# Kernel tuning notes

Measured on AMD Instinct MI355X. Metric: run time of the kernel, lower is better.

## Reference

```python
import jax, jax.numpy as jnp
import numpy as np

B, S, HID = 2, 2048, 2560
NH, NKV, HD = 8, 4, 256
Q_SIZE, KV_SIZE = NH * HD, NKV * HD
SCALE = 256.0 ** -0.5
SLIDING_WINDOW = 1024 - 1  # config.sliding_window - 1
ROPE_BASE = 10000.0
EPS = 1e-6


def rmsnorm(x, w, eps=EPS):
    xf = x.astype(jnp.float32)
    out = xf * jax.lax.rsqrt(jnp.mean(xf * xf, axis=-1, keepdims=True) + eps)
    return (out * (1.0 + w.astype(jnp.float32))).astype(x.dtype)


def apply_rope(x, positions):
    # x: [B,S,H,D], neox style (rotate halves)
    d = x.shape[-1]
    inv_freq = 1.0 / (ROPE_BASE ** (jnp.arange(0, d, 2, dtype=jnp.float32) / d))
    freqs = positions.astype(jnp.float32)[..., None] * inv_freq  # [B,S,d/2]
    cos = jnp.cos(freqs)[:, :, None, :]
    sin = jnp.sin(freqs)[:, :, None, :]
    x1, x2 = x[..., : d // 2], x[..., d // 2:]
    return jnp.concatenate([x1 * cos - x2 * sin, x2 * cos + x1 * sin], axis=-1).astype(x.dtype)


def setup_inputs() -> dict:
    key = jax.random.key(0)
    ks = jax.random.split(key, 4)
    positions = jnp.broadcast_to(jnp.arange(S, dtype=jnp.int32)[None, :], (B, S))
    hidden_states = jax.random.normal(ks[0], (B, S, HID), dtype=jnp.float32)
    attention_mask = jnp.ones((B, S), dtype=jnp.int32)
    Wqkv = jax.random.normal(ks[1], (HID, Q_SIZE + 2 * KV_SIZE), dtype=jnp.float32) * (HID ** -0.5)
    Wo = jax.random.normal(ks[2], (Q_SIZE, HID), dtype=jnp.float32) * (Q_SIZE ** -0.5)
    q_norm_w = jnp.zeros((HD,), dtype=jnp.float32)
    k_norm_w = jnp.zeros((HD,), dtype=jnp.float32)
    return {"positions": positions, "hidden_states": hidden_states,
            "attention_mask": attention_mask, "Wqkv": Wqkv, "Wo": Wo,
            "q_norm_w": q_norm_w, "k_norm_w": k_norm_w}


def reference(positions, hidden_states, attention_mask, Wqkv, Wo, q_norm_w, k_norm_w):
    b, s, _ = hidden_states.shape
    qkv = hidden_states @ Wqkv
    q, k, v = jnp.split(qkv, [Q_SIZE, Q_SIZE + KV_SIZE], axis=-1)
    q = q.reshape(b, s, NH, HD)
    k = k.reshape(b, s, NKV, HD)
    v = v.reshape(b, s, NKV, HD)
    q = rmsnorm(q, q_norm_w)
    k = rmsnorm(k, k_norm_w)
    q = apply_rope(q, positions)
    k = apply_rope(k, positions)

    # additive mask, replicating source exactly
    idx = jnp.arange(s)
    causal = idx[None, :] > idx[:, None]             # triu(diag=1)
    too_far = (idx[None, :] - idx[:, None]) > SLIDING_WINDOW
    base_mask = causal | too_far                      # [S,S]
    key_pad = attention_mask.astype(bool) == False    # [B,S]
    masked = base_mask[None, None, :, :] | key_pad[:, None, None, :]  # [B,1,S,S]
    add_mask = jnp.where(masked, -jnp.inf, 0.0).astype(jnp.float32)

    # GQA: group queries over kv heads
    g = NH // NKV
    qg = q.reshape(b, s, NKV, g, HD)
    scores = jnp.einsum('bsmgd,btmd->bmgst', qg, k) * SCALE  # [B,NKV,g,S,S]
    scores = scores + add_mask[:, :, None, :, :]
    probs = jax.nn.softmax(scores, axis=-1)
    out = jnp.einsum('bmgst,btmd->bsmgd', probs, v)           # [B,S,NKV,g,HD]
    out = out.reshape(b, s, NH * HD)
    return out @ Wo
```

## Files before the change

kernel.cpp:

```cpp
#include <hip/hip_runtime.h>
#include <stdint.h>

#define S_LEN 2048
#define BATCH 2
#define HIDDEN 2560
#define NH 8
#define NKV 4
#define HD 256
#define QSZ (NH*HD)
#define NQKV 4096
#define MROWS (BATCH*S_LEN)
#define SCALE_ATT 0.0625f

using bf16x8 = __attribute__((__ext_vector_type__(8))) __bf16;
using f32x4  = __attribute__((__ext_vector_type__(4))) float;
using s16x8  = __attribute__((__ext_vector_type__(8))) short;

union B8u { s16x8 s; bf16x8 b; };
union I4B8 { int4 i; bf16x8 b; };

__device__ __forceinline__ unsigned short f2bf(float x){
  unsigned u = __float_as_uint(x);
  u += 0x7fffu + ((u >> 16) & 1u);
  return (unsigned short)(u >> 16);
}
__device__ __forceinline__ float bf2f(unsigned short h){
  return __uint_as_float(((unsigned)h) << 16);
}
__device__ __forceinline__ bf16x8 ld_bf8(const unsigned short* p){
  B8u u; u.s = *reinterpret_cast<const s16x8*>(p); return u.b;
}
__device__ __forceinline__ f32x4 mfma16(bf16x8 a, bf16x8 b, f32x4 c){
  return __builtin_amdgcn_mfma_f32_16x16x32_bf16(a, b, c, 0, 0, 0);
}
__device__ __forceinline__ void gload16(const void* g, void* l){
  __builtin_amdgcn_global_load_lds((const __attribute__((address_space(1))) void*)g,
                                   (__attribute__((address_space(3))) void*)l,
                                   16, 0, 0);
}
__device__ __forceinline__ int cvtpk(float lo, float hi){
  int r;
  asm("v_cvt_pk_bf16_f32 %0, %1, %2" : "=v"(r) : "v"(lo), "v"(hi));
  return r;
}

__global__ __launch_bounds__(256) void cast_bf16_kernel(
    const float* __restrict__ in, unsigned short* __restrict__ out, int n)
{
  int i = (blockIdx.x * 256 + threadIdx.x) * 4;
  if (i < n){
    float4 v = *reinterpret_cast<const float4*>(in + i);
    ushort4 o;
    o.x = f2bf(v.x); o.y = f2bf(v.y); o.z = f2bf(v.z); o.w = f2bf(v.w);
    *reinterpret_cast<ushort4*>(out + i) = o;
  }
}

__global__ __launch_bounds__(256) void tcast_kernel(
    const float* __restrict__ in, unsigned short* __restrict__ out, int R, int C)
{
  __shared__ float t[32][33];
  int c0 = blockIdx.x * 32, r0 = blockIdx.y * 32;
  int tx = threadIdx.x & 31, ty = threadIdx.x >> 5;
#pragma unroll
  for (int ii = 0; ii < 4; ii++)
    t[ty + ii*8][tx] = in[(size_t)(r0 + ty + ii*8) * C + c0 + tx];
  __syncthreads();
#pragma unroll
  for (int ii = 0; ii < 4; ii++)
    out[(size_t)(c0 + ty + ii*8) * R + r0 + tx] = f2bf(t[tx][ty + ii*8]);
}

template<int BF16OUT>
__global__ __launch_bounds__(512, 2) void gemm256_kernel(
    const unsigned short* __restrict__ A,
    const unsigned short* __restrict__ BT,
    void* __restrict__ Cv,
    int N, int K, int nbn)
{
  __shared__ unsigned short Ab[2][256 * 64];
  __shared__ unsigned short Bb[2][256 * 64];

  const int tid  = threadIdx.x;
  const int lane = tid & 63;
  const int wid  = tid >> 6;
  const int wm = wid >> 2, wn = wid & 3;
  const int lq = lane & 15, lk = lane >> 4;

  const int cpx = gridDim.x >> 3;
  const int wg  = (blockIdx.x & 7) * cpx + (blockIdx.x >> 3);
  const int bm = wg / nbn, bn = wg % nbn;

  const int l8 = lane >> 3;
  const int sl = ((lane & 7) ^ l8) * 8;
  const unsigned short* agS = A  + (size_t)(bm*256 + wid*16 + l8) * K + sl;
  const unsigned short* bgS = BT + (size_t)(bn*256 + wid*16 + l8) * K + sl;

  f32x4 acc[4][4][2] = {};
  bf16x8 a[4][2], b[2][2];

#define STA(c, h, tt) do {                                                    \
    unsigned short* d = &Ab[c][(h)*8192 + wid*1024];                          \
    const unsigned short* s = agS + (size_t)(h)*128*K + (size_t)(tt)*64;      \
    gload16(s, d); gload16(s + 8*(size_t)K, d + 512);                         \
  } while (0)
#define STB(c, h, tt) do {                                                    \
    unsigned short* d = &Bb[c][(h)*8192 + wid*1024];                          \
    const unsigned short* s = bgS + (size_t)(h)*128*K + (size_t)(tt)*64;      \
    gload16(s, d); gload16(s + 8*(size_t)K, d + 512);                         \
  } while (0)
#define LDA(qa) do {                                                          \
    _Pragma("unroll") for (int m = 0; m < 4; m++)                             \
    _Pragma("unroll") for (int kk = 0; kk < 2; kk++)                          \
      a[m][kk] = ld_bf8(&Ab[cur][((qa)*128 + wm*64 + m*16 + lq)*64            \
                                 + (((kk*4 + lk) ^ (lq & 7)) << 3)]);         \
  } while (0)
#define LDB(qb) do {                                                          \
    _Pragma("unroll") for (int n = 0; n < 2; n++)                             \
    _Pragma("unroll") for (int kk = 0; kk < 2; kk++)                          \
      b[n][kk] = ld_bf8(&Bb[cur][((qb)*128 + wn*32 + n*16 + lq)*64            \
                                 + (((kk*4 + lk) ^ (lq & 7)) << 3)]);         \
  } while (0)
#define MM(qi) do {                                                           \
    __builtin_amdgcn_s_setprio(1);                                            \
    _Pragma("unroll") for (int m = 0; m < 4; m++)                             \
    _Pragma("unroll") for (int n = 0; n < 2; n++)                             \
    _Pragma("unroll") for (int kk = 0; kk < 2; kk++)                          \
      acc[qi][m][n] = mfma16(a[m][kk], b[n][kk], acc[qi][m][n]);              \
    __builtin_amdgcn_s_setprio(0);                                            \
  } while (0)
#define BARR __builtin_amdgcn_s_barrier()
#define VM(n) asm volatile("s_waitcnt vmcnt(" #n ")" ::: "memory")

  STA(0, 0, 0); STB(0, 0, 0); STB(0, 1, 0); STA(0, 1, 0);
  VM(4); BARR;

  const int NT = K >> 6;
  for (int t = 0; t < NT - 1; ++t){
    const int cur = t & 1, nxt = cur ^ 1;
    LDA(0); LDB(0); STA(nxt, 0, t+1);
    BARR; MM(0); VM(4); BARR;
    LDB(1);         STB(nxt, 0, t+1);
    BARR; MM(1); VM(4); BARR;
    LDA(1);         STB(nxt, 1, t+1);
    BARR; MM(2);        BARR;
    LDB(0);         STA(nxt, 1, t+1);
    BARR; MM(3); VM(4); BARR;
  }
  {
    const int cur = (NT - 1) & 1;
    LDA(0); LDB(0); BARR; MM(0); VM(2); BARR;
    LDB(1);         BARR; MM(1); VM(0); BARR;
    LDA(1);         BARR; MM(2);        BARR;
    LDB(0);         BARR; MM(3);        BARR;
  }
#undef STA
#undef STB
#undef LDA
#undef LDB
#undef MM
#undef BARR
#undef VM

#pragma unroll
  for (int qi = 0; qi < 4; qi++){
    const int qa = qi >> 1;
    const int qb = (qi ^ (qi >> 1)) & 1;
    const int r0 = bm*256 + qa*128 + wm*64;
    const int c0 = bn*256 + qb*128 + wn*32;
#pragma unroll
    for (int m = 0; m < 4; m++)
#pragma unroll
      for (int n = 0; n < 2; n++)
#pragma unroll
        for (int i = 0; i < 4; i++){
          const size_t idx = (size_t)(r0 + m*16 + lk*4 + i) * N + (c0 + n*16 + lq);
          if (BF16OUT) ((unsigned short*)Cv)[idx] = f2bf(acc[qi][m][n][i]);
          else         ((float*)Cv)[idx]          = acc[qi][m][n][i];
        }
  }
}

__global__ __launch_bounds__(256) void normrope_kernel(
    const unsigned short* __restrict__ qkv,
    const int* __restrict__ positions,
    const float* __restrict__ qw, const float* __restrict__ kw,
    unsigned short* __restrict__ qB,
    unsigned short* __restrict__ kB,
    unsigned short* __restrict__ vT)
{
  const int s = blockIdx.x, b = blockIdx.y;
  const int lane = threadIdx.x & 63, wid = threadIdx.x >> 6;
  const unsigned short* row = qkv + (size_t)(b * S_LEN + s) * NQKV;
  const float fpos = (float)positions[b * S_LEN + s];

#pragma unroll
  for (int t = 0; t < 4; t++){
    const int seg = t * 4 + wid;
    const int base = seg * HD;
    float x0 = bf2f(row[base + lane]);
    float x1 = bf2f(row[base + lane + 64]);
    float x2 = bf2f(row[base + lane + 128]);
    float x3 = bf2f(row[base + lane + 192]);
    if (seg >= 12){
      const int mh = seg - 12;
      unsigned short* vb = vT + (size_t)(b * NKV + mh) * HD * S_LEN + s;
      vb[(size_t)(lane      ) * S_LEN] = f2bf(x0);
      vb[(size_t)(lane +  64) * S_LEN] = f2bf(x1);
      vb[(size_t)(lane + 128) * S_LEN] = f2bf(x2);
      vb[(size_t)(lane + 192) * S_LEN] = f2bf(x3);
    } else {
      const float* w = (seg < 8) ? qw : kw;
      float ssq = x0*x0 + x1*x1 + x2*x2 + x3*x3;
#pragma unroll
      for (int d = 1; d < 64; d <<= 1) ssq += __shfl_xor(ssq, d, 64);
      float rs = rsqrtf(ssq * (1.0f / 256.0f) + 1e-6f);
      float y0 = x0 * rs * (1.0f + w[lane]);
      float y1 = x1 * rs * (1.0f + w[lane + 64]);
      float y2 = x2 * rs * (1.0f + w[lane + 128]);
      float y3 = x3 * rs * (1.0f + w[lane + 192]);
      const float kln = -9.210340371976184f / 128.0f;
      float inv1 = expf((float)lane * kln);
      float inv2 = expf((float)(lane + 64) * kln);
      float s1, c1, s2, c2;
      sincosf(fpos * inv1, &s1, &c1);
      sincosf(fpos * inv2, &s2, &c2);
      float o0 = y0 * c1 - y2 * s1;
      float o2 = y2 * c1 + y0 * s1;
      float o1 = y1 * c2 - y3 * s2;
      float o3 = y3 * c2 + y1 * s2;
      unsigned short* dst = (seg < 8)
        ? qB + ((size_t)(b * NH  +  seg     ) * S_LEN + s) * HD
        : kB + ((size_t)(b * NKV + (seg - 8)) * S_LEN + s) * HD;
      dst[lane      ] = f2bf(o0);
      dst[lane +  64] = f2bf(o1);
      dst[lane + 128] = f2bf(o2);
      dst[lane + 192] = f2bf(o3);
    }
  }
}

__global__ void maskbits_kernel(const int* __restrict__ amask, unsigned* __restrict__ bm,
                                int* __restrict__ ctr)
{
  int t = threadIdx.x;
  int b = t >> 6, tile = t & 63;
  unsigned m = 0;
  for (int j = 0; j < 32; j++)
    m |= (amask[b * S_LEN + tile * 32 + j] != 0 ? 1u : 0u) << j;
  bm[t] = m;
  if (t < 8) ctr[t] = 0;
}

__global__ __launch_bounds__(256) void attn_kernel(
    const unsigned short* __restrict__ qB,
    const unsigned short* __restrict__ kB,
    const unsigned short* __restrict__ vT,
    const unsigned* __restrict__ bmG,
    unsigned short* __restrict__ attnO,
    int* __restrict__ ctr)
{
  __shared__ unsigned short Kb[4][32 * 256];
  __shared__ unsigned short Vb[4][256 * 32];
  __shared__ unsigned bm_lds[64];
  __shared__ int s_idx;

  const int tid  = threadIdx.x;
  const int lane = tid & 63, wid = tid >> 6;
  const int c  = blockIdx.x & 7;
  const int mh = c & 3, b = c >> 2;
  const int h  = mh * 2 + (wid >> 1);
  const int lq = lane & 15, lk = lane >> 4;

  if (tid < 64) bm_lds[tid] = bmG[(b << 6) + tid];

  const unsigned short* kbase = kB + (size_t)(b * NKV + mh) * S_LEN * HD;
  const unsigned short* vbase = vT + (size_t)(b * NKV + mh) * HD * S_LEN;
  const int krow0 = wid * 2 + (lane >> 5);
  const int kgsrc = (lane & 31) ^ (krow0 & 7);
  const unsigned short* kg0 = kbase + (size_t)krow0 * HD + kgsrc * 8;
  const int vd0 = wid * 16 + (lane >> 2);
  const int vgsrc = (lane & 3) ^ ((lane >> 3) & 3);
  const unsigned short* vg0 = vbase + (size_t)vd0 * S_LEN + vgsrc * 8;

#define STAGE_K(buf, ktv)                                                      \
  do {                                                                         \
    _Pragma("unroll")                                                          \
    for (int r = 0; r < 4; r++)                                                \
      gload16(kg0 + (size_t)(ktv) * HD + r * (8 * HD),                         \
              &Kb[buf][wid * 512 + r * 2048]);                                 \
  } while (0)
#define STAGE_V(buf, ktv)                                                      \
  do {                                                                         \
    _Pragma("unroll")                                                          \
    for (int r = 0; r < 4; r++)                                                \
      gload16(vg0 + (ktv) + (size_t)r * (64 * S_LEN),                          \
              &Vb[buf][wid * 512 + r * 2048]);                                 \
  } while (0)

  for (;;){
    if (tid == 0) s_idx = atomicAdd(&ctr[c], 1);
    __syncthreads();
    const int idx = s_idx;
    __syncthreads();
    if (idx >= 64) break;
    const int qt = 63 - idx;

    const int q0 = qt * 32 + (wid & 1) * 16;
    const int q  = q0 + lq;

    const unsigned short* qbase = qB + ((size_t)(b * NH + h) * S_LEN + q0 + lq) * HD + lk * 8;
    bf16x8 aq[8];
#pragma unroll
    for (int ks = 0; ks < 8; ks++) aq[ks] = ld_bf8(qbase + ks * 32);
    asm volatile("s_waitcnt vmcnt(0)" ::: "memory");

    float mi = -__builtin_inff(), li = 0.f;
    f32x4 oacc[16] = {};

    STAGE_K(0, 0); STAGE_V(0, 0);
    if (qt >= 1){ STAGE_K(1, 32); STAGE_V(1, 32); }
    if (qt >= 2){ STAGE_K(2, 64); STAGE_V(2, 64); }
    if (qt >= 3){ STAGE_K(3, 96); STAGE_V(3, 96); }

    const int npairs = (qt >> 1) + 1;
    for (int p = 0; p < npairs; ++p){
      const int ktA = p * 64;
      const int ktB = ktA + 32;
      const bool hasB = (2*p + 1 <= qt);
      const int bufA = (2*p) & 3, bufB = (2*p + 1) & 3;

      const int ahead = qt - 2*p - 1;
      if (ahead >= 2)      asm volatile("s_waitcnt vmcnt(16)" ::: "memory");
      else if (ahead == 1) asm volatile("s_waitcnt vmcnt(8)"  ::: "memory");
      else                 asm volatile("s_waitcnt vmcnt(0)"  ::: "memory");
      __syncthreads();

      f32x4 sA0 = {0.f,0.f,0.f,0.f}, sA1 = {0.f,0.f,0.f,0.f};
      f32x4 sB0 = {0.f,0.f,0.f,0.f}, sB1 = {0.f,0.f,0.f,0.f};
      if (hasB){
#pragma unroll
        for (int ks = 0; ks < 8; ks++){
          const int slot = (((ks * 4 + lk) ^ (lq & 7)) << 3);
          bf16x8 kA0 = ld_bf8(&Kb[bufA][lq * 256 + slot]);
          bf16x8 kA1 = ld_bf8(&Kb[bufA][(16 + lq) * 256 + slot]);
          bf16x8 kB0 = ld_bf8(&Kb[bufB][lq * 256 + slot]);
          bf16x8 kB1 = ld_bf8(&Kb[bufB][(16 + lq) * 256 + slot]);
          sA0 = mfma16(kA0, aq[ks], sA0);
          sA1 = mfma16(kA1, aq[ks], sA1);
          sB0 = mfma16(kB0, aq[ks], sB0);
          sB1 = mfma16(kB1, aq[ks], sB1);
        }
      } else {
#pragma unroll
        for (int ks = 0; ks < 8; ks++){
          const int slot = (((ks * 4 + lk) ^ (lq & 7)) << 3);
          bf16x8 kA0 = ld_bf8(&Kb[bufA][lq * 256 + slot]);
          bf16x8 kA1 = ld_bf8(&Kb[bufA][(16 + lq) * 256 + slot]);
          sA0 = mfma16(kA0, aq[ks], sA0);
          sA1 = mfma16(kA1, aq[ks], sA1);
        }
      }

      const unsigned mA = bm_lds[ktA >> 5];
      const unsigned mB = bm_lds[(ktB >> 5) & 63];
      const int koff = lk * 4;
      float vA0[4], vA1[4], vB0[4], vB1[4];
#pragma unroll
      for (int j2 = 0; j2 < 4; j2++){
        const bool a0 = (ktA + koff + j2 <= q)      && ((mA >> (koff + j2)) & 1u);
        const bool a1 = (ktA + 16 + koff + j2 <= q) && ((mA >> (16 + koff + j2)) & 1u);
        vA0[j2] = a0 ? sA0[j2] * SCALE_ATT : -__builtin_inff();
        vA1[j2] = a1 ? sA1[j2] * SCALE_ATT : -__builtin_inff();
      }
      if (hasB){
#pragma unroll
        for (int j2 = 0; j2 < 4; j2++){
          const bool b0 = (ktB + koff + j2 <= q)      && ((mB >> (koff + j2)) & 1u);
          const bool b1 = (ktB + 16 + koff + j2 <= q) && ((mB >> (16 + koff + j2)) & 1u);
          vB0[j2] = b0 ? sB0[j2] * SCALE_ATT : -__builtin_inff();
          vB1[j2] = b1 ? sB1[j2] * SCALE_ATT : -__builtin_inff();
        }
      } else {
#pragma unroll
        for (int j2 = 0; j2 < 4; j2++){ vB0[j2] = -__builtin_inff(); vB1[j2] = -__builtin_inff(); }
      }
      float tm = fmaxf(fmaxf(fmaxf(vA0[0], vA0[1]), fmaxf(vA0[2], vA0[3])),
                       fmaxf(fmaxf(vA1[0], vA1[1]), fmaxf(vA1[2], vA1[3])));
      if (hasB){
        float tb = fmaxf(fmaxf(fmaxf(vB0[0], vB0[1]), fmaxf(vB0[2], vB0[3])),
                         fmaxf(fmaxf(vB1[0], vB1[1]), fmaxf(vB1[2], vB1[3])));
        tm = fmaxf(tm, tb);
      }
      tm = fmaxf(tm, __shfl_xor(tm, 16, 64));
      tm = fmaxf(tm, __shfl_xor(tm, 32, 64));

      float pA0[4], pA1[4], pB0[4], pB1[4];
      if (__all(tm <= mi + 8.0f)){
        const float mns = fmaxf(mi, -1e30f);
#pragma unroll
        for (int j2 = 0; j2 < 4; j2++){
          pA0[j2] = __expf(vA0[j2] - mns); pA1[j2] = __expf(vA1[j2] - mns);
          pB0[j2] = __expf(vB0[j2] - mns); pB1[j2] = __expf(vB1[j2] - mns);
        }
        float rs = (pA0[0]+pA0[1])+(pA0[2]+pA0[3])+(pA1[0]+pA1[1])+(pA1[2]+pA1[3])
                 + (pB0[0]+pB0[1])+(pB0[2]+pB0[3])+(pB1[0]+pB1[1])+(pB1[2]+pB1[3]);
        rs += __shfl_xor(rs, 16, 64);
        rs += __shfl_xor(rs, 32, 64);
        li += rs;
      } else {
        const float mn  = fmaxf(mi, tm);
        const float mns = fmaxf(mn, -1e30f);
#pragma unroll
        for (int j2 = 0; j2 < 4; j2++){
          pA0[j2] = __expf(vA0[j2] - mns); pA1[j2] = __expf(vA1[j2] - mns);
          pB0[j2] = __expf(vB0[j2] - mns); pB1[j2] = __expf(vB1[j2] - mns);
        }
        const float a_ = __expf(mi - mns);
        float rs = (pA0[0]+pA0[1])+(pA0[2]+pA0[3])+(pA1[0]+pA1[1])+(pA1[2]+pA1[3])
                 + (pB0[0]+pB0[1])+(pB0[2]+pB0[3])+(pB1[0]+pB1[1])+(pB1[2]+pB1[3]);
        rs += __shfl_xor(rs, 16, 64);
        rs += __shfl_xor(rs, 32, 64);
        li = li * a_ + rs;
        mi = mn;
        float av[4];
#pragma unroll
        for (int i = 0; i < 4; i++)
          av[i] = __shfl(a_, (lane & 48) | (lk * 4 + i), 64);
#pragma unroll
        for (int db = 0; db < 16; db++){
          f32x4 o = oacc[db];
#pragma unroll
          for (int i = 0; i < 4; i++) o[i] *= av[i];
          oacc[db] = o;
        }
      }

      const int sA_ = (((lk & 1) * 2) << 4) | lq;
      const int sB_ = sA_ + 16;
      const bool hi = (lk >= 2);
      I4B8 pauA, pauB;
      {
        const int w0 = cvtpk(pA0[0], pA0[1]), w1 = cvtpk(pA0[2], pA0[3]);
        const int w2 = cvtpk(pA1[0], pA1[1]), w3 = cvtpk(pA1[2], pA1[3]);
        const int a0 = __shfl(w0, sA_, 64), a1 = __shfl(w1, sA_, 64);
        const int b0 = __shfl(w0, sB_, 64), b1 = __shfl(w1, sB_, 64);
        const int c0w = __shfl(w2, sA_, 64), c1w = __shfl(w3, sA_, 64);
        const int d0w = __shfl(w2, sB_, 64), d1w = __shfl(w3, sB_, 64);
        pauA.i.x = hi ? c0w : a0;
        pauA.i.y = hi ? c1w : a1;
        pauA.i.z = hi ? d0w : b0;
        pauA.i.w = hi ? d1w : b1;
      }
      if (hasB){
        const int w0 = cvtpk(pB0[0], pB0[1]), w1 = cvtpk(pB0[2], pB0[3]);
        const int w2 = cvtpk(pB1[0], pB1[1]), w3 = cvtpk(pB1[2], pB1[3]);
        const int a0 = __shfl(w0, sA_, 64), a1 = __shfl(w1, sA_, 64);
        const int b0 = __shfl(w0, sB_, 64), b1 = __shfl(w1, sB_, 64);
        const int c0w = __shfl(w2, sA_, 64), c1w = __shfl(w3, sA_, 64);
        const int d0w = __shfl(w2, sB_, 64), d1w = __shfl(w3, sB_, 64);
        pauB.i.x = hi ? c0w : a0;
        pauB.i.y = hi ? c1w : a1;
        pauB.i.z = hi ? d0w : b0;
        pauB.i.w = hi ? d1w : b1;
      }

      const int vslot = (lk ^ ((lq >> 1) & 3)) << 3;
      if (hasB){
#pragma unroll
        for (int db = 0; db < 16; db++){
          bf16x8 vfA = ld_bf8(&Vb[bufA][(db * 16 + lq) * 32 + vslot]);
          bf16x8 vfB = ld_bf8(&Vb[bufB][(db * 16 + lq) * 32 + vslot]);
          f32x4 o = mfma16(pauA.b, vfA, oacc[db]);
          oacc[db] = mfma16(pauB.b, vfB, o);
        }
      } else {
#pragma unroll
        for (int db = 0; db < 16; db++){
          bf16x8 vfA = ld_bf8(&Vb[bufA][(db * 16 + lq) * 32 + vslot]);
          oacc[db] = mfma16(pauA.b, vfA, oacc[db]);
        }
      }

      __syncthreads();
      if (2*p + 4 <= qt){ STAGE_K(bufA, ktA + 128); STAGE_V(bufA, ktA + 128); }
      if (2*p + 5 <= qt){ STAGE_K(bufB, ktB + 128); STAGE_V(bufB, ktB + 128); }
    }

#pragma unroll
    for (int i = 0; i < 4; i++){
      const float lf = __shfl(li, (lane & 48) | (lk * 4 + i), 64);
      const float inv = 1.0f / lf;
      unsigned short* orow = attnO + (size_t)(b * S_LEN + q0 + lk*4 + i) * QSZ + h * HD + lq;
#pragma unroll
      for (int db = 0; db < 16; db++)
        orow[db * 16] = f2bf(oacc[db][i] * inv);
    }
  }
#undef STAGE_K
#undef STAGE_V
}

extern "C" void kernel_launch(void* const* d_in, const int* in_sizes, int n_in,
                              void* d_out, int out_size, void* d_ws, size_t ws_size,
                              hipStream_t stream)
{
  const int*   positions = (const int*)  d_in[0];
  const float* hidden    = (const float*)d_in[1];
  const int*   amask     = (const int*)  d_in[2];
  const float* Wqkv      = (const float*)d_in[3];
  const float* Wo        = (const float*)d_in[4];
  const float* qw        = (const float*)d_in[5];
  const float* kw        = (const float*)d_in[6];
  float* out = (float*)d_out;

  char* ws = (char*)d_ws;
  unsigned short* hB    = (unsigned short*)(ws);
  unsigned short* attnO = (unsigned short*)(ws);
  unsigned short* WqT   = (unsigned short*)(ws + 20971520);
  unsigned short* WoT   = (unsigned short*)(ws + 41943040);
  unsigned short* qkvB  = (unsigned short*)(ws + 52428800);
  unsigned short* qb    = (unsigned short*)(ws + 119537664);
  unsigned short* kb    = (unsigned short*)(ws + 136314880);
  unsigned short* vt    = (unsigned short*)(ws + 144703488);
  unsigned*       bm    = (unsigned*)     (ws + 153092096);
  int*            ctr   = (int*)          (ws + 153092608);

  cast_bf16_kernel<<<dim3(MROWS * HIDDEN / 1024), 256, 0, stream>>>(hidden, hB, MROWS * HIDDEN);
  tcast_kernel<<<dim3(NQKV / 32, HIDDEN / 32), 256, 0, stream>>>(Wqkv, WqT, HIDDEN, NQKV);
  tcast_kernel<<<dim3(HIDDEN / 32, QSZ / 32), 256, 0, stream>>>(Wo, WoT, QSZ, HIDDEN);
  maskbits_kernel<<<dim3(1), 128, 0, stream>>>(amask, bm, ctr);

  gemm256_kernel<1><<<dim3((MROWS/256) * (NQKV/256)), 512, 0, stream>>>(
      hB, WqT, qkvB, NQKV, HIDDEN, NQKV/256);

  normrope_kernel<<<dim3(S_LEN, BATCH), 256, 0, stream>>>(qkvB, positions, qw, kw, qb, kb, vt);

  attn_kernel<<<dim3(256), 256, 0, stream>>>(qb, kb, vt, bm, attnO, ctr);

  gemm256_kernel<0><<<dim3((MROWS/256) * (HIDDEN/256)), 512, 0, stream>>>(
      attnO, WoT, out, HIDDEN, QSZ, HIDDEN/256);
}
```

Before: 336.4 us.

## Fuse QK RMSNorm, RoPE and V transpose into QKV GEMM epilogue

Removes the separate normrope kernel and the bf16 qkv intermediate. The QKV GEMM epilogue now computes per-row RMS across a 256-wide head tile through an LDS reduction, applies RoPE from a precomputed cos/sin table, and writes q/k/v^T directly. A small ropetab kernel builds the sin/cos tables, and the epilogue stores are scattered 2-byte writes with strided table reads. The goal is to cut a full round trip through memory and a kernel launch, at the cost of a heavier epilogue and more register pressure.

```diff
diff --git a/kernel.cpp b/kernel.cpp
--- a/kernel.cpp
+++ b/kernel.cpp
@@ -24,9 +24,6 @@
   u += 0x7fffu + ((u >> 16) & 1u);
   return (unsigned short)(u >> 16);
 }
-__device__ __forceinline__ float bf2f(unsigned short h){
-  return __uint_as_float(((unsigned)h) << 16);
-}
 __device__ __forceinline__ bf16x8 ld_bf8(const unsigned short* p){
   B8u u; u.s = *reinterpret_cast<const s16x8*>(p); return u.b;
 }
@@ -71,16 +68,38 @@
     out[(size_t)(c0 + ty + ii*8) * R + r0 + tx] = f2bf(t[tx][ty + ii*8]);
 }
 
-template<int BF16OUT>
-__global__ __launch_bounds__(512, 2) void gemm256_kernel(
+__global__ __launch_bounds__(256) void ropetab_kernel(
+    const int* __restrict__ positions, float* __restrict__ ct, float* __restrict__ st)
+{
+  const int cix = blockIdx.x;
+  const int b   = blockIdx.y;
+  const float kln = -9.210340371976184f / 128.0f;
+  const float inv = expf((float)cix * kln);
+  float* cp = ct + ((size_t)b * 128 + cix) * 2048;
+  float* sp = st + ((size_t)b * 128 + cix) * 2048;
+  for (int s = threadIdx.x; s < S_LEN; s += 256){
+    float fpos = (float)positions[b * S_LEN + s];
+    float sv, cv;
+    sincosf(fpos * inv, &sv, &cv);
+    cp[s] = cv;
+    sp[s] = sv;
+  }
+}
+
+__global__ __launch_bounds__(512, 2) void gemm_qkv_kernel(
     const unsigned short* __restrict__ A,
     const unsigned short* __restrict__ BT,
-    void* __restrict__ Cv,
-    int N, int K, int nbn)
+    const float* __restrict__ qw, const float* __restrict__ kw,
+    const float* __restrict__ ct, const float* __restrict__ st,
+    unsigned short* __restrict__ qB,
+    unsigned short* __restrict__ kB,
+    unsigned short* __restrict__ vT)
 {
   __shared__ unsigned short Ab[2][256 * 64];
   __shared__ unsigned short Bb[2][256 * 64];
 
+  const int K = HIDDEN;
+  const int nbn = 16;
   const int tid  = threadIdx.x;
   const int lane = tid & 63;
   const int wid  = tid >> 6;
@@ -162,6 +181,199 @@
 #undef BARR
 #undef VM
 
+  __syncthreads();
+  const int b_  = bm >> 3;
+  const int sb0 = (bm & 7) * 256;
+
+  if (bn >= 12){
+    const int mhv = bn - 12;
+#pragma unroll
+    for (int qi = 0; qi < 4; qi++){
+      const int qa = qi >> 1, qb = (qi ^ (qi >> 1)) & 1;
+#pragma unroll
+      for (int m = 0; m < 4; m++){
+        const int s0 = sb0 + qa*128 + wm*64 + m*16 + lk*4;
+#pragma unroll
+        for (int n = 0; n < 2; n++){
+          const int d = qb*128 + wn*32 + n*16 + lq;
+          ushort4 o;
+          o.x = f2bf(acc[qi][m][n][0]);
+          o.y = f2bf(acc[qi][m][n][1]);
+          o.z = f2bf(acc[qi][m][n][2]);
+          o.w = f2bf(acc[qi][m][n][3]);
+          *reinterpret_cast<ushort4*>(
+              vT + ((size_t)((b_*NKV + mhv)*HD + d))*S_LEN + s0) = o;
+        }
+      }
+    }
+  } else {
+    float* red = (float*)Ab;
+    float part[2][4][4];
+#pragma unroll
+    for (int qa = 0; qa < 2; qa++){
+      const int qiA = qa ? 3 : 0, qiB = qa ? 2 : 1;
+#pragma unroll
+      for (int m = 0; m < 4; m++)
+#pragma unroll
+      for (int i = 0; i < 4; i++){
+        float s = 0.f;
+#pragma unroll
+        for (int n = 0; n < 2; n++)
+          s += acc[qiA][m][n][i]*acc[qiA][m][n][i]
+             + acc[qiB][m][n][i]*acc[qiB][m][n][i];
+        s += __shfl_xor(s, 1, 64);
+        s += __shfl_xor(s, 2, 64);
+        s += __shfl_xor(s, 4, 64);
+        s += __shfl_xor(s, 8, 64);
+        part[qa][m][i] = s;
+      }
+    }
+    if (lq == 0){
+#pragma unroll
+      for (int qa = 0; qa < 2; qa++)
+#pragma unroll
+      for (int m = 0; m < 4; m++)
+#pragma unroll
+      for (int i = 0; i < 4; i++)
+        red[wn*256 + qa*128 + wm*64 + m*16 + lk*4 + i] = part[qa][m][i];
+    }
+    __syncthreads();
+    float rsv[2][4][4];
+#pragma unroll
+    for (int qa = 0; qa < 2; qa++)
+#pragma unroll
+    for (int m = 0; m < 4; m++)
+#pragma unroll
+    for (int i = 0; i < 4; i++){
+      const int row = qa*128 + wm*64 + m*16 + lk*4 + i;
+      float tt = red[row] + red[256 + row] + red[512 + row] + red[768 + row];
+      rsv[qa][m][i] = rsqrtf(tt * (1.0f/256.0f) + 1e-6f);
+    }
+    const float* wv = (bn < 8) ? qw : kw;
+    unsigned short* dstB = (bn < 8)
+      ? qB + ((size_t)(b_*NH  + bn      ) * S_LEN) * HD
+      : kB + ((size_t)(b_*NKV + (bn - 8)) * S_LEN) * HD;
+    const float* ctb = ct + (size_t)b_ * 128 * 2048;
+    const float* stb = st + (size_t)b_ * 128 * 2048;
+#pragma unroll
+    for (int qa = 0; qa < 2; qa++){
+      const int qiA = qa ? 3 : 0, qiB = qa ? 2 : 1;
+#pragma unroll
+      for (int m = 0; m < 4; m++){
+        const int s0 = sb0 + qa*128 + wm*64 + m*16 + lk*4;
+#pragma unroll
+        for (int n = 0; n < 2; n++){
+          const int c0 = wn*32 + n*16 + lq;
+          const float w0 = 1.0f + wv[c0];
+          const float w1 = 1.0f + wv[c0 + 128];
+          const float4 c4 = *reinterpret_cast<const float4*>(ctb + (size_t)c0*2048 + s0);
+          const float4 s4 = *reinterpret_cast<const float4*>(stb + (size_t)c0*2048 + s0);
+#pragma unroll
+          for (int i = 0; i < 4; i++){
+            const float rs_ = rsv[qa][m][i];
+            const float y0 = acc[qiA][m][n][i] * rs_ * w0;
+            const float y1 = acc[qiB][m][n][i] * rs_ * w1;
+            const float cc = (&c4.x)[i], ss = (&s4.x)[i];
+            unsigned short* p = dstB + (size_t)(s0 + i) * HD;
+            p[c0]       = f2bf(y0 * cc - y1 * ss);
+            p[c0 + 128] = f2bf(y1 * cc + y0 * ss);
+          }
+        }
+      }
+    }
+  }
+}
+
+__global__ __launch_bounds__(512, 2) void gemm256_kernel(
+    const unsigned short* __restrict__ A,
+    const unsigned short* __restrict__ BT,
+    float* __restrict__ C,
+    int N, int K, int nbn)
+{
+  __shared__ unsigned short Ab[2][256 * 64];
+  __shared__ unsigned short Bb[2][256 * 64];
+
+  const int tid  = threadIdx.x;
+  const int lane = tid & 63;
+  const int wid  = tid >> 6;
+  const int wm = wid >> 2, wn = wid & 3;
+  const int lq = lane & 15, lk = lane >> 4;
+
+  const int cpx = gridDim.x >> 3;
+  const int wg  = (blockIdx.x & 7) * cpx + (blockIdx.x >> 3);
+  const int bm = wg / nbn, bn = wg % nbn;
+
+  const int l8 = lane >> 3;
+  const int sl = ((lane & 7) ^ l8) * 8;
+  const unsigned short* agS = A  + (size_t)(bm*256 + wid*16 + l8) * K + sl;
+  const unsigned short* bgS = BT + (size_t)(bn*256 + wid*16 + l8) * K + sl;
+
+  f32x4 acc[4][4][2] = {};
+  bf16x8 a[4][2], b[2][2];
+
+#define STA(c, h, tt) do {                                                    \
+    unsigned short* d = &Ab[c][(h)*8192 + wid*1024];                          \
+    const unsigned short* s = agS + (size_t)(h)*128*K + (size_t)(tt)*64;      \
+    gload16(s, d); gload16(s + 8*(size_t)K, d + 512);                         \
+  } while (0)
+#define STB(c, h, tt) do {                                                    \
+    unsigned short* d = &Bb[c][(h)*8192 + wid*1024];                          \
+    const unsigned short* s = bgS + (size_t)(h)*128*K + (size_t)(tt)*64;      \
+    gload16(s, d); gload16(s + 8*(size_t)K, d + 512);                         \
+  } while (0)
+#define LDA(qa) do {                                                          \
+    _Pragma("unroll") for (int m = 0; m < 4; m++)                             \
+    _Pragma("unroll") for (int kk = 0; kk < 2; kk++)                          \
+      a[m][kk] = ld_bf8(&Ab[cur][((qa)*128 + wm*64 + m*16 + lq)*64            \
+                                 + (((kk*4 + lk) ^ (lq & 7)) << 3)]);         \
+  } while (0)
+#define LDB(qb) do {                                                          \
+    _Pragma("unroll") for (int n = 0; n < 2; n++)                             \
+    _Pragma("unroll") for (int kk = 0; kk < 2; kk++)                          \
+      b[n][kk] = ld_bf8(&Bb[cur][((qb)*128 + wn*32 + n*16 + lq)*64            \
+                                 + (((kk*4 + lk) ^ (lq & 7)) << 3)]);         \
+  } while (0)
+#define MM(qi) do {                                                           \
+    __builtin_amdgcn_s_setprio(1);                                            \
+    _Pragma("unroll") for (int m = 0; m < 4; m++)                             \
+    _Pragma("unroll") for (int n = 0; n < 2; n++)                             \
+    _Pragma("unroll") for (int kk = 0; kk < 2; kk++)                          \
+      acc[qi][m][n] = mfma16(a[m][kk], b[n][kk], acc[qi][m][n]);              \
+    __builtin_amdgcn_s_setprio(0);                                            \
+  } while (0)
+#define BARR __builtin_amdgcn_s_barrier()
+#define VM(n) asm volatile("s_waitcnt vmcnt(" #n ")" ::: "memory")
+
+  STA(0, 0, 0); STB(0, 0, 0); STB(0, 1, 0); STA(0, 1, 0);
+  VM(4); BARR;
+
+  const int NT = K >> 6;
+  for (int t = 0; t < NT - 1; ++t){
+    const int cur = t & 1, nxt = cur ^ 1;
+    LDA(0); LDB(0); STA(nxt, 0, t+1);
+    BARR; MM(0); VM(4); BARR;
+    LDB(1);         STB(nxt, 0, t+1);
+    BARR; MM(1); VM(4); BARR;
+    LDA(1);         STB(nxt, 1, t+1);
+    BARR; MM(2);        BARR;
+    LDB(0);         STA(nxt, 1, t+1);
+    BARR; MM(3); VM(4); BARR;
+  }
+  {
+    const int cur = (NT - 1) & 1;
+    LDA(0); LDB(0); BARR; MM(0); VM(2); BARR;
+    LDB(1);         BARR; MM(1); VM(0); BARR;
+    LDA(1);         BARR; MM(2);        BARR;
+    LDB(0);         BARR; MM(3);        BARR;
+  }
+#undef STA
+#undef STB
+#undef LDA
+#undef LDB
+#undef MM
+#undef BARR
+#undef VM
+
 #pragma unroll
   for (int qi = 0; qi < 4; qi++){
     const int qa = qi >> 1;
@@ -173,70 +385,8 @@
 #pragma unroll
       for (int n = 0; n < 2; n++)
 #pragma unroll
-        for (int i = 0; i < 4; i++){
-          const size_t idx = (size_t)(r0 + m*16 + lk*4 + i) * N + (c0 + n*16 + lq);
-          if (BF16OUT) ((unsigned short*)Cv)[idx] = f2bf(acc[qi][m][n][i]);
-          else         ((float*)Cv)[idx]          = acc[qi][m][n][i];
-        }
-  }
-}
-
-__global__ __launch_bounds__(256) void normrope_kernel(
-    const unsigned short* __restrict__ qkv,
-    const int* __restrict__ positions,
-    const float* __restrict__ qw, const float* __restrict__ kw,
-    unsigned short* __restrict__ qB,
-    unsigned short* __restrict__ kB,
-    unsigned short* __restrict__ vT)
-{
-  const int s = blockIdx.x, b = blockIdx.y;
-  const int lane = threadIdx.x & 63, wid = threadIdx.x >> 6;
-  const unsigned short* row = qkv + (size_t)(b * S_LEN + s) * NQKV;
-  const float fpos = (float)positions[b * S_LEN + s];
-
-#pragma unroll
-  for (int t = 0; t < 4; t++){
-    const int seg = t * 4 + wid;
-    const int base = seg * HD;
-    float x0 = bf2f(row[base + lane]);
-    float x1 = bf2f(row[base + lane + 64]);
-    float x2 = bf2f(row[base + lane + 128]);
-    float x3 = bf2f(row[base + lane + 192]);
-    if (seg >= 12){
-      const int mh = seg - 12;
-      unsigned short* vb = vT + (size_t)(b * NKV + mh) * HD * S_LEN + s;
-      vb[(size_t)(lane      ) * S_LEN] = f2bf(x0);
-      vb[(size_t)(lane +  64) * S_LEN] = f2bf(x1);
-      vb[(size_t)(lane + 128) * S_LEN] = f2bf(x2);
-      vb[(size_t)(lane + 192) * S_LEN] = f2bf(x3);
-    } else {
-      const float* w = (seg < 8) ? qw : kw;
-      float ssq = x0*x0 + x1*x1 + x2*x2 + x3*x3;
-#pragma unroll
-      for (int d = 1; d < 64; d <<= 1) ssq += __shfl_xor(ssq, d, 64);
-      float rs = rsqrtf(ssq * (1.0f / 256.0f) + 1e-6f);
-      float y0 = x0 * rs * (1.0f + w[lane]);
-      float y1 = x1 * rs * (1.0f + w[lane + 64]);
-      float y2 = x2 * rs * (1.0f + w[lane + 128]);
-      float y3 = x3 * rs * (1.0f + w[lane + 192]);
-      const float kln = -9.210340371976184f / 128.0f;
-      float inv1 = expf((float)lane * kln);
-      float inv2 = expf((float)(lane + 64) * kln);
-      float s1, c1, s2, c2;
-      sincosf(fpos * inv1, &s1, &c1);
-      sincosf(fpos * inv2, &s2, &c2);
-      float o0 = y0 * c1 - y2 * s1;
-      float o2 = y2 * c1 + y0 * s1;
-      float o1 = y1 * c2 - y3 * s2;
-      float o3 = y3 * c2 + y1 * s2;
-      unsigned short* dst = (seg < 8)
-        ? qB + ((size_t)(b * NH  +  seg     ) * S_LEN + s) * HD
-        : kB + ((size_t)(b * NKV + (seg - 8)) * S_LEN + s) * HD;
-      dst[lane      ] = f2bf(o0);
-      dst[lane +  64] = f2bf(o1);
-      dst[lane + 128] = f2bf(o2);
-      dst[lane + 192] = f2bf(o3);
-    }
+        for (int i = 0; i < 4; i++)
+          C[(size_t)(r0 + m*16 + lk*4 + i) * N + (c0 + n*16 + lq)] = acc[qi][m][n][i];
   }
 }
 
@@ -519,7 +669,8 @@
   unsigned short* attnO = (unsigned short*)(ws);
   unsigned short* WqT   = (unsigned short*)(ws + 20971520);
   unsigned short* WoT   = (unsigned short*)(ws + 41943040);
-  unsigned short* qkvB  = (unsigned short*)(ws + 52428800);
+  float*          ct    = (float*)        (ws + 52428800);
+  float*          st    = (float*)        (ws + 56623104);
   unsigned short* qb    = (unsigned short*)(ws + 119537664);
   unsigned short* kb    = (unsigned short*)(ws + 136314880);
   unsigned short* vt    = (unsigned short*)(ws + 144703488);
@@ -530,14 +681,13 @@
   tcast_kernel<<<dim3(NQKV / 32, HIDDEN / 32), 256, 0, stream>>>(Wqkv, WqT, HIDDEN, NQKV);
   tcast_kernel<<<dim3(HIDDEN / 32, QSZ / 32), 256, 0, stream>>>(Wo, WoT, QSZ, HIDDEN);
   maskbits_kernel<<<dim3(1), 128, 0, stream>>>(amask, bm, ctr);
-
-  gemm256_kernel<1><<<dim3((MROWS/256) * (NQKV/256)), 512, 0, stream>>>(
-      hB, WqT, qkvB, NQKV, HIDDEN, NQKV/256);
-
-  normrope_kernel<<<dim3(S_LEN, BATCH), 256, 0, stream>>>(qkvB, positions, qw, kw, qb, kb, vt);
+  ropetab_kernel<<<dim3(128, BATCH), 256, 0, stream>>>(positions, ct, st);
+
+  gemm_qkv_kernel<<<dim3((MROWS/256) * (NQKV/256)), 512, 0, stream>>>(
+      hB, WqT, qw, kw, ct, st, qb, kb, vt);
 
   attn_kernel<<<dim3(256), 256, 0, stream>>>(qb, kb, vt, bm, attnO, ctr);
 
-  gemm256_kernel<0><<<dim3((MROWS/256) * (HIDDEN/256)), 512, 0, stream>>>(
+  gemm256_kernel<<<dim3((MROWS/256) * (HIDDEN/256)), 512, 0, stream>>>(
       attnO, WoT, out, HIDDEN, QSZ, HIDDEN/256);
 }
```

New measurement: 317.7 us. 1.06x faster.
